# Kernel tuning notes

Measured on AMD Instinct MI355X. Metric: run time of the kernel, lower is better.

Reference implementation:

```python
import jax, jax.numpy as jnp
import numpy as np

B, C, T = 64, 64, 2048
HID, OUT = 256, 10
NEW_T = T // 4
N = B * NEW_T  # 32768 nodes
E = 524288


def setup_inputs() -> dict:
    key = jax.random.key(0)
    ks = jax.random.split(key, 16)
    inp = {
        "x": jax.random.normal(ks[0], (B, C, T), dtype=jnp.float32),
        "edge_index": jax.random.randint(ks[1], (2, E), 0, N, dtype=jnp.int64),
        "conv1_w": jax.random.normal(ks[2], (16, C, 5), dtype=jnp.float32) * 0.05,
        "conv1_b": jnp.zeros((16,), jnp.float32),
        "conv2_w": jax.random.normal(ks[3], (32, 16, 5), dtype=jnp.float32) * 0.1,
        "conv2_b": jnp.zeros((32,), jnp.float32),
        "gcn1_w": jax.random.normal(ks[4], (32, HID), dtype=jnp.float32) * 0.1,
        "gcn1_b": jnp.zeros((HID,), jnp.float32),
        "gcn2_w": jax.random.normal(ks[5], (HID, HID), dtype=jnp.float32) * 0.05,
        "gcn2_b": jnp.zeros((HID,), jnp.float32),
        "cls_w": jax.random.normal(ks[6], (HID, OUT), dtype=jnp.float32) * 0.05,
        "cls_b": jnp.zeros((OUT,), jnp.float32),
    }
    return inp


def _conv1d(x, w, b):
    # x: [B, Cin, T], w: [Cout, Cin, K] -> [B, Cout, T] (padding=2 for K=5)
    y = jax.lax.conv_general_dilated(
        x, w, window_strides=(1,), padding=[(2, 2)],
        dimension_numbers=("NCH", "OIH", "NCH"))
    return y + b[None, :, None]


def _maxpool2(x):
    b, c, t = x.shape
    return x.reshape(b, c, t // 2, 2).max(axis=-1)


def _gcn(x, w, bias, src, dst):
    # PyG GCNConv: add self-loops, symmetric norm D^-1/2 (A+I) D^-1/2, x@W, aggregate, +bias
    n = N
    loops = jnp.arange(n, dtype=src.dtype)
    s = jnp.concatenate([src, loops])
    d = jnp.concatenate([dst, loops])
    deg = jax.ops.segment_sum(jnp.ones_like(d, dtype=x.dtype), d, num_segments=n)
    dinv = jnp.where(deg > 0, jax.lax.rsqrt(deg), 0.0)
    norm = dinv[s] * dinv[d]  # [E+N]
    xw = x @ w  # [N, H]
    msg = xw[s] * norm[:, None]
    out = jax.ops.segment_sum(msg, d, num_segments=n)
    return out + bias


def reference(x, edge_index, conv1_w, conv1_b, conv2_w, conv2_b,
              gcn1_w, gcn1_b, gcn2_w, gcn2_b, cls_w, cls_b):
    h = _maxpool2(jax.nn.relu(_conv1d(x, conv1_w, conv1_b)))
    h = _maxpool2(jax.nn.relu(_conv1d(h, conv2_w, conv2_b)))  # [B, 32, NEW_T]
    h = h.transpose(0, 2, 1).reshape(-1, 32)  # [N, 32]
    src, dst = edge_index[0], edge_index[1]
    h = jax.nn.relu(_gcn(h, gcn1_w, gcn1_b, src, dst))
    h = jax.nn.relu(_gcn(h, gcn2_w, gcn2_b, src, dst))
    h = h.reshape(B, NEW_T, HID).mean(axis=1)  # global mean over temporal nodes
    return h @ cls_w + cls_b
```

## Files before the change

kernel.cpp:

```cpp
#include <hip/hip_runtime.h>

#define B_ 64
#define CIN 64
#define T_ 2048
#define C1 16
#define T1 1024
#define C2 32
#define T2 512
#define NN 32768
#define HID 256
#define OUTD 10
#define NE 524288
#define NTOT (NE + NN)

typedef __attribute__((ext_vector_type(4))) float fx4;
typedef __attribute__((ext_vector_type(8))) _Float16 hx8;
typedef __attribute__((ext_vector_type(4))) _Float16 hx4;
typedef __attribute__((ext_vector_type(2))) _Float16 hx2;

#define OFF_H      (0ull)
#define OFF_Z      (16ull<<20)
#define OFF_H1     (33ull<<20)
#define OFF_XN     (37ull<<20)
#define OFF_Y1     (42ull<<20)
#define OFF_DEG    (46ull<<20)
#define OFF_INDPTR ((46ull<<20) + (256u<<10))
#define OFF_CNT    ((46ull<<20) + (512u<<10))
#define OFF_DINV   ((46ull<<20) + (768u<<10))
#define OFF_CSRC   (47ull<<20)
#define OFF_WT1    (51ull<<20)
#define OFF_WT2    (OFF_WT1 + (64u<<10))
#define OFF_POOL   (OFF_WT1 + (128u<<10))
#define OFF_W2T    (OFF_WT1 + (256u<<10))

__device__ __forceinline__ fx4 shfl_xor4(fx4 v, int m) {
    return (fx4){__shfl_xor(v.x, m), __shfl_xor(v.y, m), __shfl_xor(v.z, m), __shfl_xor(v.w, m)};
}

__global__ __launch_bounds__(256) void k_setup(int* deg, int* cnt, float* pooled,
                                               const float* __restrict__ w1, const float* __restrict__ w2,
                                               float* __restrict__ wt1, float* __restrict__ wt2,
                                               const float* __restrict__ gw2, _Float16* __restrict__ w2t,
                                               unsigned* __restrict__ xnz, unsigned* __restrict__ zz) {
    __shared__ float tl[64][65];
    int blk = blockIdx.x, t = threadIdx.x;
    if (blk < 128) {
        int i = blk * 256 + t;
        if (i < NN) { deg[i] = 1; cnt[i] = 0; }
        if (i < B_ * HID) pooled[i] = 0.f;
        if (blk == 0 && t < 16) xnz[t] = 0u;
        if (blk == 1 && t < 128) zz[t] = 0u;
    } else if (blk < 144) {
        int bb = blk - 128;
        int bx = bb & 3, by = bb >> 2;
        #pragma unroll
        for (int it = 0; it < 16; it++) {
            int idx = it * 256 + t;
            int r = idx >> 6, c = idx & 63;
            tl[r][c] = gw2[(size_t)(bx * 64 + r) * 256 + by * 64 + c];
        }
        __syncthreads();
        #pragma unroll
        for (int it = 0; it < 16; it++) {
            int idx = it * 256 + t;
            int r = idx >> 6, c = idx & 63;
            w2t[(size_t)(by * 64 + r) * 256 + bx * 64 + c] = (_Float16)tl[c][r];
        }
    } else {
        int i = (blk - 144) * 256 + t;
        if (i < 16 * 64 * 5) {
            int co = i & 15; int r = i >> 4; int k = r % 5; int ci = r / 5;
            wt1[i] = w1[(co * 64 + ci) * 5 + k];
        }
        int j = i - 16 * 64 * 5;
        if (j >= 0 && j < 32 * 16 * 5) {
            int co = j & 31; int r = j >> 5; int k = r % 5; int ci = r / 5;
            wt2[j] = w2[(co * 16 + ci) * 5 + k];
        }
    }
}

__global__ __launch_bounds__(1024) void k_scan(const int* __restrict__ deg, int* __restrict__ indptr,
                                               float* __restrict__ dinv) {
    __shared__ int wsum[16];
    int tid = threadIdx.x;
    int lane = tid & 63, w = tid >> 6;
    int base = tid * 32;
    int loc[32]; int s = 0;
    #pragma unroll
    for (int j = 0; j < 32; j++) {
        int d = deg[base + j];
        dinv[base + j] = rsqrtf((float)d);
        loc[j] = d;
        s += (d + 7) & ~7;
    }
    int v = s;
    #pragma unroll
    for (int off = 1; off < 64; off <<= 1) {
        int t = __shfl_up(v, off);
        if (lane >= off) v += t;
    }
    if (lane == 63) wsum[w] = v;
    __syncthreads();
    int woff = 0;
    #pragma unroll
    for (int i = 0; i < 16; i++) { int t = wsum[i]; if (i < w) woff += t; }
    int run = woff + v - s;
    #pragma unroll
    for (int j = 0; j < 32; j++) { indptr[base + j] = run; run += (loc[j] + 7) & ~7; }
    if (tid == 1023) { indptr[NN] = run; dinv[NN] = 0.f; }
}

#define LDX 72
__global__ __launch_bounds__(256) void k_c1cnt(const float* __restrict__ x, const float* __restrict__ wt1,
                                               const float* __restrict__ b1, float* __restrict__ h1,
                                               const int* __restrict__ ei, int* __restrict__ deg) {
    int blk = blockIdx.x;
    int tid = threadIdx.x;
    if (blk >= 512) {
        int t = (blk - 512) * 256 + tid;
        int4 d4 = *(const int4*)&ei[NE + 4 * t];
        atomicAdd(&deg[d4.x], 1);
        atomicAdd(&deg[d4.y], 1);
        atomicAdd(&deg[d4.z], 1);
        atomicAdd(&deg[d4.w], 1);
        return;
    }
    __shared__ _Float16 xs[260 * LDX];
    __shared__ _Float16 wl[16 * 328];
    __shared__ float ps2[128 * 17];
    int tile = blk & 7;
    int b = blk >> 3;
    int t0 = tile * 256;
    const float* xb = x + ((size_t)b * CIN) * T_ + t0;
    {
        int f = tid & 63, r0 = tid >> 6;
        #pragma unroll
        for (int it = 0; it < 16; it++) {
            int r = r0 + 4 * it;
            fx4 v = *(const fx4*)&xb[(size_t)r * T_ + f * 4];
            #pragma unroll
            for (int q = 0; q < 4; q++) {
                int j = 2 + f * 4 + q;
                xs[j * LDX + ((((r >> 3) ^ (j >> 3)) & 7) << 3) + (r & 7)] = (_Float16)v[q];
            }
        }
        int r = tid >> 2, c = tid & 3;
        int off = (c < 2) ? (c - 2) : (254 + c);
        int gt = t0 + off;
        float v = 0.f;
        if (gt >= 0 && gt < T_) v = xb[(size_t)r * T_ + off];
        xs[(off + 2) * LDX + r] = (_Float16)v;
        for (int i = tid; i < 5120; i += 256) {
            int K = i >> 4, co = i & 15;
            int kk = K >> 6, ci = K & 63;
            wl[co * 328 + K] = (_Float16)wt1[(ci * 5 + kk) * 16 + co];
        }
    }
    __syncthreads();
    int wv = tid >> 6, lane = tid & 63;
    int l15 = lane & 15, g = lane >> 4;
    fx4 acc[4];
    #pragma unroll
    for (int m = 0; m < 4; m++) acc[m] = (fx4){0.f, 0.f, 0.f, 0.f};
    #pragma unroll
    for (int ks = 0; ks < 10; ks++) {
        int kk = ks >> 1;
        int cb = (ks & 1) * 4 + g;
        hx8 bf = *(const hx8*)&wl[l15 * 328 + ks * 32 + g * 8];
        #pragma unroll
        for (int m = 0; m < 4; m++) {
            int j = wv * 64 + m * 16 + l15 + kk;
            hx8 af = *(const hx8*)&xs[j * LDX + ((((j >> 3) & 7) ^ cb) << 3)];
            acc[m] = __builtin_amdgcn_mfma_f32_16x16x32_f16(af, bf, acc[m], 0, 0, 0);
        }
    }
    float bv = b1[l15];
    #pragma unroll
    for (int m = 0; m < 4; m++) {
        int t1b = wv * 32 + m * 8 + g * 2;
        float a0 = fmaxf(acc[m][0] + bv, 0.f);
        float a1 = fmaxf(acc[m][1] + bv, 0.f);
        float a2 = fmaxf(acc[m][2] + bv, 0.f);
        float a3 = fmaxf(acc[m][3] + bv, 0.f);
        ps2[t1b * 17 + l15] = fmaxf(a0, a1);
        ps2[(t1b + 1) * 17 + l15] = fmaxf(a2, a3);
    }
    __syncthreads();
    for (int idx = tid; idx < 2048; idx += 256) {
        int t1 = idx & 127, co = idx >> 7;
        h1[(b * C1 + co) * T1 + tile * 128 + t1] = ps2[t1 * 17 + co];
    }
}

__global__ __launch_bounds__(256) void k_c2fill(const float* __restrict__ h1, const float* __restrict__ wt2,
                                                const float* __restrict__ b2, _Float16* __restrict__ xn,
                                                const int* __restrict__ ei, const int* __restrict__ deg,
                                                const int* __restrict__ indptr, int* __restrict__ cnt,
                                                int* __restrict__ csrc) {
    int blk = blockIdx.x;
    int tid = threadIdx.x;
    if (blk >= 256) {
        int t = (blk - 256) * 256 + tid;
        if (t < NE / 4) {
            int4 s4 = *(const int4*)&ei[4 * t];
            int4 d4 = *(const int4*)&ei[NE + 4 * t];
            int p0 = indptr[d4.x] + atomicAdd(&cnt[d4.x], 1); csrc[p0] = s4.x;
            int p1 = indptr[d4.y] + atomicAdd(&cnt[d4.y], 1); csrc[p1] = s4.y;
            int p2 = indptr[d4.z] + atomicAdd(&cnt[d4.z], 1); csrc[p2] = s4.z;
            int p3 = indptr[d4.w] + atomicAdd(&cnt[d4.w], 1); csrc[p3] = s4.w;
        } else if (t < NE / 4 + NN) {
            int n = t - NE / 4;
            int pos = indptr[n] + atomicAdd(&cnt[n], 1);
            csrc[pos] = n;
        } else {
            int n = t - NE / 4 - NN;
            if (n < NN) {
                int dd = deg[n], dp = (dd + 7) & ~7, base = indptr[n];
                for (int j = dd; j < dp; j++) csrc[base + j] = NN;
            }
        }
        return;
    }
    __shared__ float xs[16][260];
    __shared__ float ps[128 * 32];
    int tile = blk & 3;
    int b = blk >> 2;
    int t0 = tile * 256;
    float acc[32];
    #pragma unroll
    for (int i = 0; i < 32; i++) acc[i] = 0.f;
    for (int idx = tid; idx < 16 * 260; idx += 256) {
        int r = idx / 260, c = idx % 260;
        int gt = t0 + c - 2;
        float v = 0.f;
        if (gt >= 0 && gt < T1) v = h1[(b * C1 + r) * T1 + gt];
        xs[r][c] = v;
    }
    __syncthreads();
    for (int ci = 0; ci < 16; ci++) {
        float xv[5];
        #pragma unroll
        for (int j = 0; j < 5; j++) xv[j] = xs[ci][tid + j];
        const float* wp = wt2 + (ci * 5) * 32;
        #pragma unroll
        for (int k = 0; k < 5; k++) {
            #pragma unroll
            for (int co = 0; co < 32; co++)
                acc[co] = fmaf(xv[k], wp[k * 32 + co], acc[co]);
        }
    }
    #pragma unroll
    for (int co = 0; co < 32; co++) {
        float a = fmaxf(acc[co] + b2[co], 0.f);
        float o = fmaxf(a, __shfl_xor(a, 1));
        if ((tid & 1) == 0) ps[(tid >> 1) * 32 + co] = o;
    }
    __syncthreads();
    size_t base = ((size_t)b * T2 + tile * 128) * 32;
    for (int idx = tid; idx < 128 * 16; idx += 256) {
        hx2 h;
        h.x = (_Float16)ps[2 * idx];
        h.y = (_Float16)ps[2 * idx + 1];
        *(hx2*)&xn[base + 2 * idx] = h;
    }
}

#define ACC4(v, m) \
    acc.x = fmaf((float)v[0], m, acc.x); acc.y = fmaf((float)v[1], m, acc.y); \
    acc.z = fmaf((float)v[2], m, acc.z); acc.w = fmaf((float)v[3], m, acc.w);

__global__ __launch_bounds__(256) void k_agg32(const _Float16* __restrict__ xn, const int* __restrict__ indptr,
                                               const int* __restrict__ csrc, const float* __restrict__ dinv,
                                               float* __restrict__ y1) {
    int lane = threadIdx.x & 63;
    int n = blockIdx.x * 4 + (threadIdx.x >> 6);
    int eg = lane >> 3, fi = lane & 7;
    int beg = indptr[n];
    int cnt8 = indptr[n + 1] - beg;
    float dn = dinv[n];
    const int* cs = csrc + beg;
    fx4 acc = (fx4){0.f, 0.f, 0.f, 0.f};
    for (int i = 0; i < cnt8; i += 8) {
        int s = cs[i + eg];
        float m = dinv[s] * dn;
        hx4 v = *(const hx4*)&xn[(size_t)s * 32 + fi * 4];
        ACC4(v, m)
    }
    acc += shfl_xor4(acc, 8);
    acc += shfl_xor4(acc, 16);
    acc += shfl_xor4(acc, 32);
    if (lane < 8) *(fx4*)&y1[(size_t)n * 32 + fi * 4] = acc;
}

__global__ __launch_bounds__(256) void k_gemm1(const float* __restrict__ A, const float* __restrict__ W,
                                               const float* __restrict__ bias, _Float16* __restrict__ H) {
    __shared__ __align__(16) float xT[32 * 68];
    __shared__ __align__(16) float wl[32 * 256];
    int tid = threadIdx.x;
    int ty = tid >> 4, tx = tid & 15;
    int rows0 = blockIdx.x * 64;
    int kq = tid & 7, rs = tid >> 3;
    {
        fx4 v0 = *(const fx4*)&A[(size_t)(rows0 + rs) * 32 + kq * 4];
        fx4 v1 = *(const fx4*)&A[(size_t)(rows0 + rs + 32) * 32 + kq * 4];
        #pragma unroll
        for (int i = 0; i < 4; i++) {
            xT[(kq * 4 + i) * 68 + rs]      = v0[i];
            xT[(kq * 4 + i) * 68 + rs + 32] = v1[i];
        }
    }
    #pragma unroll
    for (int m = 0; m < 8; m++)
        *(fx4*)&wl[m * 1024 + tid * 4] = *(const fx4*)&W[(size_t)(m * 1024 + tid * 4)];
    __syncthreads();

    fx4 c[4][4];
    #pragma unroll
    for (int i = 0; i < 4; i++)
        #pragma unroll
        for (int j = 0; j < 4; j++) c[i][j] = (fx4){0.f, 0.f, 0.f, 0.f};

    #pragma unroll 8
    for (int kk = 0; kk < 32; kk++) {
        fx4 xa = *(const fx4*)&xT[kk * 68 + ty * 4];
        fx4 w[4];
        w[0] = *(const fx4*)&wl[kk * 256 + tx * 8];
        w[1] = *(const fx4*)&wl[kk * 256 + tx * 8 + 4];
        w[2] = *(const fx4*)&wl[kk * 256 + tx * 8 + 128];
        w[3] = *(const fx4*)&wl[kk * 256 + tx * 8 + 132];
        #pragma unroll
        for (int j = 0; j < 4; j++) {
            c[0][j] += xa.x * w[j];
            c[1][j] += xa.y * w[j];
            c[2][j] += xa.z * w[j];
            c[3][j] += xa.w * w[j];
        }
    }
    fx4 bb[4];
    bb[0] = *(const fx4*)&bias[tx * 8];
    bb[1] = *(const fx4*)&bias[tx * 8 + 4];
    bb[2] = *(const fx4*)&bias[tx * 8 + 128];
    bb[3] = *(const fx4*)&bias[tx * 8 + 132];
    #pragma unroll
    for (int i = 0; i < 4; i++) {
        int r = rows0 + ty * 4 + i;
        fx4 v0 = c[i][0] + bb[0], v1 = c[i][1] + bb[1];
        fx4 v2 = c[i][2] + bb[2], v3 = c[i][3] + bb[3];
        hx8 h0, h1;
        #pragma unroll
        for (int q = 0; q < 4; q++) {
            h0[q]     = (_Float16)fmaxf(v0[q], 0.f);
            h0[q + 4] = (_Float16)fmaxf(v1[q], 0.f);
            h1[q]     = (_Float16)fmaxf(v2[q], 0.f);
            h1[q + 4] = (_Float16)fmaxf(v3[q], 0.f);
        }
        *(hx8*)&H[(size_t)r * 256 + tx * 8]       = h0;
        *(hx8*)&H[(size_t)r * 256 + tx * 8 + 128] = h1;
    }
}

#define LDH 72
__global__ __launch_bounds__(256, 2) void k_gemm2m(const _Float16* __restrict__ A,
                                                   const _Float16* __restrict__ Bt,
                                                   _Float16* __restrict__ Z) {
    __shared__ __align__(16) _Float16 As[2][128 * LDH];
    __shared__ __align__(16) _Float16 Bs[2][128 * LDH];
    int tid = threadIdx.x;
    int lane = tid & 63, wid = tid >> 6;
    int wm = wid >> 1, wn = wid & 1;
    int row0 = blockIdx.x * 128, col0 = blockIdx.y * 128;
    int l15 = lane & 15, g = lane >> 4;
    int sr = tid >> 3, sc = tid & 7;

    fx4 acc[4][4];
    #pragma unroll
    for (int m = 0; m < 4; m++)
        #pragma unroll
        for (int n = 0; n < 4; n++) acc[m][n] = (fx4){0.f, 0.f, 0.f, 0.f};

    uint4 ga[4], gb[4];
    #pragma unroll
    for (int it = 0; it < 4; it++) {
        ga[it] = *(const uint4*)&A[(size_t)(row0 + sr + 32 * it) * 256 + sc * 8];
        gb[it] = *(const uint4*)&Bt[(size_t)(col0 + sr + 32 * it) * 256 + sc * 8];
    }
    #pragma unroll
    for (int it = 0; it < 4; it++) {
        *(uint4*)&As[0][(sr + 32 * it) * LDH + sc * 8] = ga[it];
        *(uint4*)&Bs[0][(sr + 32 * it) * LDH + sc * 8] = gb[it];
    }
    __syncthreads();

    int cur = 0;
    for (int t = 0; t < 4; t++) {
        if (t < 3) {
            int k0 = (t + 1) * 64;
            #pragma unroll
            for (int it = 0; it < 4; it++) {
                ga[it] = *(const uint4*)&A[(size_t)(row0 + sr + 32 * it) * 256 + k0 + sc * 8];
                gb[it] = *(const uint4*)&Bt[(size_t)(col0 + sr + 32 * it) * 256 + k0 + sc * 8];
            }
        }
        const _Float16* ap = As[cur];
        const _Float16* bp = Bs[cur];
        hx8 af[4][2], bf[4][2];
        #pragma unroll
        for (int m = 0; m < 4; m++)
            #pragma unroll
            for (int ks = 0; ks < 2; ks++)
                af[m][ks] = *(const hx8*)&ap[(wm * 64 + m * 16 + l15) * LDH + ks * 32 + g * 8];
        #pragma unroll
        for (int n = 0; n < 4; n++)
            #pragma unroll
            for (int ks = 0; ks < 2; ks++)
                bf[n][ks] = *(const hx8*)&bp[(wn * 64 + n * 16 + l15) * LDH + ks * 32 + g * 8];
        #pragma unroll
        for (int m = 0; m < 4; m++)
            #pragma unroll
            for (int n = 0; n < 4; n++) {
                acc[m][n] = __builtin_amdgcn_mfma_f32_16x16x32_f16(af[m][0], bf[n][0], acc[m][n], 0, 0, 0);
                acc[m][n] = __builtin_amdgcn_mfma_f32_16x16x32_f16(af[m][1], bf[n][1], acc[m][n], 0, 0, 0);
            }
        if (t < 3) {
            #pragma unroll
            for (int it = 0; it < 4; it++) {
                *(uint4*)&As[cur ^ 1][(sr + 32 * it) * LDH + sc * 8] = ga[it];
                *(uint4*)&Bs[cur ^ 1][(sr + 32 * it) * LDH + sc * 8] = gb[it];
            }
        }
        __syncthreads();
        cur ^= 1;
    }

    #pragma unroll
    for (int m = 0; m < 4; m++)
        #pragma unroll
        for (int n = 0; n < 4; n++) {
            int cc = col0 + wn * 64 + n * 16 + l15;
            #pragma unroll
            for (int r = 0; r < 4; r++) {
                int rr = row0 + wm * 64 + m * 16 + g * 4 + r;
                Z[(size_t)rr * 256 + cc] = (_Float16)acc[m][n][r];
            }
        }
}

__global__ __launch_bounds__(256) void k_aggm(const _Float16* __restrict__ Z, const int* __restrict__ indptr,
                                              const int* __restrict__ csrc, const float* __restrict__ dinv,
                                              const float* __restrict__ bias, float* __restrict__ pooled) {
    __shared__ float ps[4][256];
    int tid = threadIdx.x;
    int wid = tid >> 6, lane = tid & 63;
    int n0 = blockIdx.x * 32 + wid * 8;
    fx4 bb = *(const fx4*)&bias[lane * 4];
    fx4 racc = (fx4){0.f, 0.f, 0.f, 0.f};
    #pragma unroll 1
    for (int u = 0; u < 8; u++) {
        int n = n0 + u;
        int beg = indptr[n];
        int cnt8 = indptr[n + 1] - beg;
        float dn = dinv[n];
        const int* cs = csrc + beg;
        fx4 acc = (fx4){0.f, 0.f, 0.f, 0.f};
        for (int i = 0; i < cnt8; i += 8) {
            int4 ia = *(const int4*)&cs[i];
            int4 ib = *(const int4*)&cs[i + 4];
            float m0 = dinv[ia.x] * dn, m1 = dinv[ia.y] * dn;
            float m2 = dinv[ia.z] * dn, m3 = dinv[ia.w] * dn;
            float m4 = dinv[ib.x] * dn, m5 = dinv[ib.y] * dn;
            float m6 = dinv[ib.z] * dn, m7 = dinv[ib.w] * dn;
            hx4 v0 = *(const hx4*)&Z[(size_t)ia.x * 256 + lane * 4];
            hx4 v1 = *(const hx4*)&Z[(size_t)ia.y * 256 + lane * 4];
            hx4 v2 = *(const hx4*)&Z[(size_t)ia.z * 256 + lane * 4];
            hx4 v3 = *(const hx4*)&Z[(size_t)ia.w * 256 + lane * 4];
            hx4 v4 = *(const hx4*)&Z[(size_t)ib.x * 256 + lane * 4];
            hx4 v5 = *(const hx4*)&Z[(size_t)ib.y * 256 + lane * 4];
            hx4 v6 = *(const hx4*)&Z[(size_t)ib.z * 256 + lane * 4];
            hx4 v7 = *(const hx4*)&Z[(size_t)ib.w * 256 + lane * 4];
            ACC4(v0, m0)
            ACC4(v1, m1)
            ACC4(v2, m2)
            ACC4(v3, m3)
            ACC4(v4, m4)
            ACC4(v5, m5)
            ACC4(v6, m6)
            ACC4(v7, m7)
        }
        acc += bb;
        racc.x += fmaxf(acc.x, 0.f); racc.y += fmaxf(acc.y, 0.f);
        racc.z += fmaxf(acc.z, 0.f); racc.w += fmaxf(acc.w, 0.f);
    }
    *(fx4*)&ps[wid][lane * 4] = racc;
    __syncthreads();
    float s = ps[0][tid] + ps[1][tid] + ps[2][tid] + ps[3][tid];
    atomicAdd(&pooled[(blockIdx.x >> 4) * 256 + tid], s * (1.f / 512.f));
}

__global__ __launch_bounds__(64) void k_cls(const float* __restrict__ pooled, const float* __restrict__ cw,
                                            const float* __restrict__ cb, float* __restrict__ outp) {
    int b = blockIdx.x, lane = threadIdx.x;
    float po[10];
    #pragma unroll
    for (int o = 0; o < 10; o++) po[o] = 0.f;
    #pragma unroll
    for (int m = 0; m < 4; m++) {
        int hh = lane + m * 64;
        float ph = pooled[b * HID + hh];
        #pragma unroll
        for (int o = 0; o < 10; o++) po[o] = fmaf(ph, cw[hh * 10 + o], po[o]);
    }
    #pragma unroll
    for (int off = 32; off >= 1; off >>= 1) {
        #pragma unroll
        for (int o = 0; o < 10; o++) po[o] += __shfl_down(po[o], off);
    }
    if (lane == 0) {
        #pragma unroll
        for (int o = 0; o < 10; o++) outp[b * 10 + o] = po[o] + cb[o];
    }
}

extern "C" void kernel_launch(void* const* d_in, const int* in_sizes, int n_in,
                              void* d_out, int out_size, void* d_ws, size_t ws_size,
                              hipStream_t stream) {
    const float* x   = (const float*)d_in[0];
    const int*   ei  = (const int*)d_in[1];
    const float* w1  = (const float*)d_in[2];
    const float* b1  = (const float*)d_in[3];
    const float* w2  = (const float*)d_in[4];
    const float* b2  = (const float*)d_in[5];
    const float* g1w = (const float*)d_in[6];
    const float* g1b = (const float*)d_in[7];
    const float* g2w = (const float*)d_in[8];
    const float* g2b = (const float*)d_in[9];
    const float* cw  = (const float*)d_in[10];
    const float* cb  = (const float*)d_in[11];
    float* out = (float*)d_out;
    char* ws = (char*)d_ws;

    _Float16*       H      = (_Float16*)(ws + OFF_H);
    _Float16*       Z      = (_Float16*)(ws + OFF_Z);
    float*          h1     = (float*)(ws + OFF_H1);
    _Float16*       xn     = (_Float16*)(ws + OFF_XN);
    float*          y1     = (float*)(ws + OFF_Y1);
    int*            deg    = (int*)(ws + OFF_DEG);
    int*            indptr = (int*)(ws + OFF_INDPTR);
    int*            cnt    = (int*)(ws + OFF_CNT);
    float*          dinv   = (float*)(ws + OFF_DINV);
    int*            csrc   = (int*)(ws + OFF_CSRC);
    float*          wt1    = (float*)(ws + OFF_WT1);
    float*          wt2    = (float*)(ws + OFF_WT2);
    float*          pooled = (float*)(ws + OFF_POOL);
    _Float16*       w2t    = (_Float16*)(ws + OFF_W2T);
    unsigned*       xnz    = (unsigned*)(xn + (size_t)NN * 32);
    unsigned*       zz     = (unsigned*)(Z + (size_t)NN * 256);

    k_setup <<<174, 256, 0, stream>>>(deg, cnt, pooled, w1, w2, wt1, wt2, g2w, w2t, xnz, zz);
    k_c1cnt <<<1024, 256, 0, stream>>>(x, wt1, b1, h1, ei, deg);
    k_scan  <<<1, 1024, 0, stream>>>(deg, indptr, dinv);
    k_c2fill<<<1280, 256, 0, stream>>>(h1, wt2, b2, xn, ei, deg, indptr, cnt, csrc);
    k_agg32 <<<8192, 256, 0, stream>>>(xn, indptr, csrc, dinv, y1);
    k_gemm1 <<<512, 256, 0, stream>>>(y1, g1w, g1b, H);
    k_gemm2m<<<dim3(256, 2), 256, 0, stream>>>(H, w2t, Z);
    k_aggm  <<<1024, 256, 0, stream>>>(Z, indptr, csrc, dinv, g2b, pooled);
    k_cls   <<<64, 64, 0, stream>>>(pooled, cw, cb, out);
}
```

Measured before the change: 176.1 us.

## Partition CSR fill by destination range per block group and pad conv2 shared buffer

The CSR scatter now launches 1088 fill blocks arranged as 8 destination groups of 4096 nodes. Each block scans a chunk of edges and handles only the destinations in its group, so atomics and csrc writes from concurrent blocks land in a narrower address range and should get better L2/cache locality. The cost is that every edge chunk is read 8 times. Self-loop insertion and padding are merged into the same loop. The conv2 pooled shared buffer is also padded to a stride of 33 to avoid LDS bank conflicts on the per-channel writes.

```diff
diff --git a/kernel.cpp b/kernel.cpp
--- a/kernel.cpp
+++ b/kernel.cpp
@@ -201,29 +201,33 @@
     int blk = blockIdx.x;
     int tid = threadIdx.x;
     if (blk >= 256) {
-        int t = (blk - 256) * 256 + tid;
-        if (t < NE / 4) {
-            int4 s4 = *(const int4*)&ei[4 * t];
-            int4 d4 = *(const int4*)&ei[NE + 4 * t];
-            int p0 = indptr[d4.x] + atomicAdd(&cnt[d4.x], 1); csrc[p0] = s4.x;
-            int p1 = indptr[d4.y] + atomicAdd(&cnt[d4.y], 1); csrc[p1] = s4.y;
-            int p2 = indptr[d4.z] + atomicAdd(&cnt[d4.z], 1); csrc[p2] = s4.z;
-            int p3 = indptr[d4.w] + atomicAdd(&cnt[d4.w], 1); csrc[p3] = s4.w;
-        } else if (t < NE / 4 + NN) {
-            int n = t - NE / 4;
-            int pos = indptr[n] + atomicAdd(&cnt[n], 1);
-            csrc[pos] = n;
-        } else {
-            int n = t - NE / 4 - NN;
-            if (n < NN) {
-                int dd = deg[n], dp = (dd + 7) & ~7, base = indptr[n];
-                for (int j = dd; j < dp; j++) csrc[base + j] = NN;
+        int j = blk - 256;
+        int g = j & 7, i = j >> 3;
+        int q0 = i * 964;
+        int q1 = (q0 + 964 < NE / 4) ? (q0 + 964) : (NE / 4);
+        for (int q = q0 + tid; q < q1; q += 256) {
+            int4 s4 = *(const int4*)&ei[4 * q];
+            int4 d4 = *(const int4*)&ei[NE + 4 * q];
+            if ((d4.x >> 12) == g) { int p = indptr[d4.x] + atomicAdd(&cnt[d4.x], 1); csrc[p] = s4.x; }
+            if ((d4.y >> 12) == g) { int p = indptr[d4.y] + atomicAdd(&cnt[d4.y], 1); csrc[p] = s4.y; }
+            if ((d4.z >> 12) == g) { int p = indptr[d4.z] + atomicAdd(&cnt[d4.z], 1); csrc[p] = s4.z; }
+            if ((d4.w >> 12) == g) { int p = indptr[d4.w] + atomicAdd(&cnt[d4.w], 1); csrc[p] = s4.w; }
+        }
+        int n0 = i * 241;
+        int n1 = (n0 + 241 < NN) ? (n0 + 241) : NN;
+        for (int n = n0 + tid; n < n1; n += 256) {
+            if ((n >> 12) == g) {
+                int base = indptr[n];
+                int p = base + atomicAdd(&cnt[n], 1);
+                csrc[p] = n;
+                int dd = deg[n], dp = (dd + 7) & ~7;
+                for (int k = dd; k < dp; k++) csrc[base + k] = NN;
             }
         }
         return;
     }
     __shared__ float xs[16][260];
-    __shared__ float ps[128 * 32];
+    __shared__ float ps[128 * 33];
     int tile = blk & 3;
     int b = blk >> 2;
     int t0 = tile * 256;
@@ -254,15 +258,16 @@
     for (int co = 0; co < 32; co++) {
         float a = fmaxf(acc[co] + b2[co], 0.f);
         float o = fmaxf(a, __shfl_xor(a, 1));
-        if ((tid & 1) == 0) ps[(tid >> 1) * 32 + co] = o;
+        if ((tid & 1) == 0) ps[(tid >> 1) * 33 + co] = o;
     }
     __syncthreads();
     size_t base = ((size_t)b * T2 + tile * 128) * 32;
     for (int idx = tid; idx < 128 * 16; idx += 256) {
+        int t1 = idx >> 4, co = (idx & 15) * 2;
         hx2 h;
-        h.x = (_Float16)ps[2 * idx];
-        h.y = (_Float16)ps[2 * idx + 1];
-        *(hx2*)&xn[base + 2 * idx] = h;
+        h.x = (_Float16)ps[t1 * 33 + co];
+        h.y = (_Float16)ps[t1 * 33 + co + 1];
+        *(hx2*)&xn[base + t1 * 32 + co] = h;
     }
 }
 
@@ -559,7 +564,7 @@
     k_setup <<<174, 256, 0, stream>>>(deg, cnt, pooled, w1, w2, wt1, wt2, g2w, w2t, xnz, zz);
     k_c1cnt <<<1024, 256, 0, stream>>>(x, wt1, b1, h1, ei, deg);
     k_scan  <<<1, 1024, 0, stream>>>(deg, indptr, dinv);
-    k_c2fill<<<1280, 256, 0, stream>>>(h1, wt2, b2, xn, ei, deg, indptr, cnt, csrc);
+    k_c2fill<<<1344, 256, 0, stream>>>(h1, wt2, b2, xn, ei, deg, indptr, cnt, csrc);
     k_agg32 <<<8192, 256, 0, stream>>>(xn, indptr, csrc, dinv, y1);
     k_gemm1 <<<512, 256, 0, stream>>>(y1, g1w, g1b, H);
     k_gemm2m<<<dim3(256, 2), 256, 0, stream>>>(H, w2t, Z);
```

Measured after the change: 166.1 us. 5.6% less time.
